# Optimization experiments

Hardware: AMD Instinct MI355X
Metric: run time of the kernel (lower is better)

## Reference

```python
import jax, jax.numpy as jnp
import numpy as np

NUM_HEADS = 16


def setup_inputs() -> dict:
    key = jax.random.key(0)
    ks = jax.random.split(key, 4)
    B, S, D = 2, 2048, 1024
    scale = 1.0 / np.sqrt(D)
    x = jax.random.normal(ks[0], (B, S, D), dtype=jnp.float32)
    Wq = jax.random.normal(ks[1], (D, D), dtype=jnp.float32) * scale
    Wk = jax.random.normal(ks[2], (D, D), dtype=jnp.float32) * scale
    Wv = jax.random.normal(ks[3], (D, D), dtype=jnp.float32) * scale
    bq = jnp.zeros((D,), dtype=jnp.float32)
    bk = jnp.zeros((D,), dtype=jnp.float32)
    bv = jnp.zeros((D,), dtype=jnp.float32)
    return {"x": x, "Wq": Wq, "bq": bq, "Wk": Wk, "bk": bk, "Wv": Wv, "bv": bv}


def _split_heads(t, H):
    B, S, D = t.shape
    return t.reshape(B, S, H, D // H).transpose(0, 2, 1, 3)  # (B,H,S,depth)


def reference(x, Wq, bq, Wk, bk, Wv, bv):
    H = NUM_HEADS
    B, S, D = x.shape
    depth = D // H
    q = _split_heads(x @ Wq + bq, H)
    k = _split_heads(x @ Wk + bk, H)
    v = _split_heads(x @ Wv + bv, H)
    # causal mask: strictly-upper-triangular ones, added as finfo.min * mask
    mask = 1.0 - jnp.tril(jnp.ones((S, S), dtype=jnp.float32))
    scores = jnp.einsum("bhqd,bhkd->bhqk", q, k) / jnp.sqrt(jnp.float32(depth))
    scores = scores + jnp.float32(np.finfo(np.float32).min) * mask
    probs = jax.nn.softmax(scores, axis=-1)
    att = jnp.einsum("bhqk,bhkd->bhqd", probs, v)
    return att.transpose(0, 2, 1, 3).reshape(B, S, D)
```

## Files before the change

### kernel.cpp

```cpp
#include <hip/hip_runtime.h>
#include <hip/hip_bf16.h>

#define B_ 2
#define S_ 2048
#define D_ 1024
#define H_ 16
#define DH 64
#define M_ (B_*S_)
#define NT_ (S_/64)

using bf16x8 = __attribute__((ext_vector_type(8))) __bf16;
using f32x4  = __attribute__((ext_vector_type(4))) float;

__device__ __forceinline__ int swz(int row) { return ((row ^ (row >> 3)) & 7) << 3; }

__device__ __forceinline__ void glds16(const __bf16* g, __bf16* l) {
#if __has_builtin(__builtin_amdgcn_global_load_lds)
  __builtin_amdgcn_global_load_lds(
      (const __attribute__((address_space(1))) unsigned int*)g,
      (__attribute__((address_space(3))) unsigned int*)l, 16, 0, 0);
#else
  *(bf16x8*)l = *(const bf16x8*)g;
#endif
}

__global__ __launch_bounds__(256) void conv_x(const float* __restrict__ x,
                                              __bf16* __restrict__ xb) {
  int idx = blockIdx.x * 256 + threadIdx.x;
  int m = idx >> 7, k = (idx & 127) * 8;
  float4 a = *(const float4*)&x[(size_t)m * D_ + k];
  float4 b = *(const float4*)&x[(size_t)m * D_ + k + 4];
  bf16x8 o;
  o[0]=(__bf16)a.x; o[1]=(__bf16)a.y; o[2]=(__bf16)a.z; o[3]=(__bf16)a.w;
  o[4]=(__bf16)b.x; o[5]=(__bf16)b.y; o[6]=(__bf16)b.z; o[7]=(__bf16)b.w;
  *(bf16x8*)&xb[(size_t)m * D_ + (k & ~63) + ((k & 63) ^ swz(m))] = o;
}

__global__ __launch_bounds__(256) void conv_w(const float* __restrict__ Wq,
                                              const float* __restrict__ Wk,
                                              const float* __restrict__ Wv,
                                              __bf16* __restrict__ wt) {
  int z = blockIdx.z;
  const float* __restrict__ W = (z == 0) ? Wq : (z == 1) ? Wk : Wv;
  __bf16* __restrict__ Wt = wt + (size_t)z * D_ * D_;
  __shared__ __bf16 Lt[64 * 66];
  int tid = threadIdx.x;
  int k0 = blockIdx.x * 64, n0 = blockIdx.y * 64;
  #pragma unroll
  for (int i = 0; i < 4; ++i) {
    int f4 = i * 256 + tid;
    int r = f4 >> 4, c4 = (f4 & 15) * 4;
    float4 v = *(const float4*)&W[(size_t)(k0 + r) * D_ + n0 + c4];
    Lt[(c4 + 0) * 66 + r] = (__bf16)v.x;
    Lt[(c4 + 1) * 66 + r] = (__bf16)v.y;
    Lt[(c4 + 2) * 66 + r] = (__bf16)v.z;
    Lt[(c4 + 3) * 66 + r] = (__bf16)v.w;
  }
  __syncthreads();
  #pragma unroll
  for (int i = 0; i < 2; ++i) {
    int idx = i * 256 + tid;
    int n = idx >> 3, kc = (idx & 7) * 8;
    int nf = n0 + n;
    bf16x8 o;
    #pragma unroll
    for (int j = 0; j < 8; ++j) o[j] = Lt[n * 66 + kc + j];
    *(bf16x8*)&Wt[(size_t)nf * D_ + k0 + (kc ^ swz(nf))] = o;
  }
}

__global__ __launch_bounds__(256) void qkv_gemm(
    const __bf16* __restrict__ xb, const __bf16* __restrict__ wt,
    const float* __restrict__ bq, const float* __restrict__ bk,
    const float* __restrict__ bv, __bf16* __restrict__ qkv) {
  int z = blockIdx.z;
  const __bf16* __restrict__ Wt = wt + (size_t)z * D_ * D_;
  const float* __restrict__ bias = (z == 0) ? bq : (z == 1) ? bk : bv;
  __bf16* __restrict__ out = qkv + (size_t)z * M_ * D_;
  const float scale = (z == 0) ? 0.125f : 1.0f;

  __shared__ __bf16 Al[128 * 64];
  __shared__ __bf16 Bl[128 * 64];

  int tid = threadIdx.x, lane = tid & 63, w = tid >> 6;
  int m0 = blockIdx.y * 128, n0 = blockIdx.x * 128;
  int wr = (w >> 1) * 64, wc = (w & 1) * 64;

  f32x4 acc[4][4] = {};

  for (int kt = 0; kt < D_ / 64; ++kt) {
    int k0 = kt * 64;
    #pragma unroll
    for (int r = 0; r < 4; ++r) {
      int e = (r * 256 + tid) * 8;
      int row = e >> 6, col = e & 63;
      glds16(&xb[(size_t)(m0 + row) * D_ + k0 + col], &Al[e]);
      glds16(&Wt[(size_t)(n0 + row) * D_ + k0 + col], &Bl[e]);
    }
    __syncthreads();

    bf16x8 af[4][2], bfr[4][2];
    #pragma unroll
    for (int mi = 0; mi < 4; ++mi) {
      int row = wr + mi * 16 + (lane & 15);
      int sr = swz(row);
      #pragma unroll
      for (int kk = 0; kk < 2; ++kk)
        af[mi][kk] = *(const bf16x8*)&Al[row * 64 + ((kk * 32 + (lane >> 4) * 8) ^ sr)];
    }
    #pragma unroll
    for (int ni = 0; ni < 4; ++ni) {
      int col = wc + ni * 16 + (lane & 15);
      int sc = swz(col);
      #pragma unroll
      for (int kk = 0; kk < 2; ++kk)
        bfr[ni][kk] = *(const bf16x8*)&Bl[col * 64 + ((kk * 32 + (lane >> 4) * 8) ^ sc)];
    }
    __builtin_amdgcn_s_setprio(1);
    #pragma unroll
    for (int kk = 0; kk < 2; ++kk)
      #pragma unroll
      for (int mi = 0; mi < 4; ++mi)
        #pragma unroll
        for (int ni = 0; ni < 4; ++ni)
          acc[mi][ni] = __builtin_amdgcn_mfma_f32_16x16x32_bf16(
              af[mi][kk], bfr[ni][kk], acc[mi][ni], 0, 0, 0);
    __builtin_amdgcn_s_setprio(0);
    __syncthreads();
  }

  #pragma unroll
  for (int mi = 0; mi < 4; ++mi) {
    #pragma unroll
    for (int ni = 0; ni < 4; ++ni) {
      int col = n0 + wc + ni * 16 + (lane & 15);
      int h = col >> 6, dh = col & 63;
      float bv_ = bias[col];
      #pragma unroll
      for (int r = 0; r < 4; ++r) {
        int row = m0 + wr + mi * 16 + (lane >> 4) * 4 + r;
        int b = row >> 11, s = row & 2047;
        out[((size_t)(b * H_ + h) * S_ + s) * DH + dh] =
            (__bf16)((acc[mi][ni][r] + bv_) * scale);
      }
    }
  }
}

__device__ __forceinline__ void attn_tile(
    const bf16x8* aq, f32x4* accO, float* mrow, float* lrow,
    const __bf16* __restrict__ Kl, const __bf16* __restrict__ Vt,
    __bf16* __restrict__ Plw, int lane, int kv0, int qbase, int diag) {
  f32x4 sf[4];
  __builtin_amdgcn_s_setprio(1);
  #pragma unroll
  for (int f = 0; f < 4; ++f) {
    f32x4 zz = {};
    int col = f * 16 + (lane & 15);
    int sc = swz(col);
    #pragma unroll
    for (int kk = 0; kk < 2; ++kk) {
      bf16x8 bk = *(const bf16x8*)&Kl[col * 64 + ((kk * 32 + (lane >> 4) * 8) ^ sc)];
      zz = __builtin_amdgcn_mfma_f32_16x16x32_bf16(aq[kk], bk, zz, 0, 0, 0);
    }
    sf[f] = zz;
  }
  __builtin_amdgcn_s_setprio(0);

  if (diag) {
    #pragma unroll
    for (int f = 0; f < 4; ++f) {
      int kvg = kv0 + f * 16 + (lane & 15);
      #pragma unroll
      for (int r = 0; r < 4; ++r) {
        int qg = qbase + (lane >> 4) * 4 + r;
        if (kvg > qg) sf[f][r] = -1e30f;
      }
    }
  }

  float alpha[4];
  #pragma unroll
  for (int r = 0; r < 4; ++r) {
    float mx = fmaxf(fmaxf(sf[0][r], sf[1][r]), fmaxf(sf[2][r], sf[3][r]));
    #pragma unroll
    for (int off = 8; off >= 1; off >>= 1)
      mx = fmaxf(mx, __shfl_xor(mx, off, 64));
    float mnew = fmaxf(mrow[r], mx);
    alpha[r] = __expf(mrow[r] - mnew);
    mrow[r] = mnew;
    float rs = 0.f;
    #pragma unroll
    for (int f = 0; f < 4; ++f) {
      float p = __expf(sf[f][r] - mnew);
      sf[f][r] = p;
      rs += p;
    }
    #pragma unroll
    for (int off = 8; off >= 1; off >>= 1)
      rs += __shfl_xor(rs, off, 64);
    lrow[r] = lrow[r] * alpha[r] + rs;
  }

  #pragma unroll
  for (int f = 0; f < 4; ++f)
    #pragma unroll
    for (int r = 0; r < 4; ++r) {
      int row = (lane >> 4) * 4 + r;
      Plw[row * 64 + ((f * 16 + (lane & 15)) ^ swz(row))] = (__bf16)sf[f][r];
    }

  #pragma unroll
  for (int f = 0; f < 4; ++f)
    #pragma unroll
    for (int r = 0; r < 4; ++r)
      accO[f][r] *= alpha[r];

  __builtin_amdgcn_s_setprio(1);
  #pragma unroll
  for (int kk = 0; kk < 2; ++kk) {
    int prow = lane & 15;
    bf16x8 pa = *(const bf16x8*)&Plw[prow * 64 + ((kk * 32 + (lane >> 4) * 8) ^ swz(prow))];
    #pragma unroll
    for (int f = 0; f < 4; ++f) {
      int vrow = f * 16 + (lane & 15);
      bf16x8 vb = *(const bf16x8*)&Vt[vrow * 64 + ((kk * 32 + (lane >> 4) * 8) ^ swz(vrow))];
      accO[f] = __builtin_amdgcn_mfma_f32_16x16x32_bf16(pa, vb, accO[f], 0, 0, 0);
    }
  }
  __builtin_amdgcn_s_setprio(0);
}

__device__ __forceinline__ void attn_out(
    const f32x4* accO, const float* lrow, float* __restrict__ out,
    int b, int h, int qbase, int lane) {
  #pragma unroll
  for (int f = 0; f < 4; ++f) {
    int dh = f * 16 + (lane & 15);
    #pragma unroll
    for (int r = 0; r < 4; ++r) {
      int qg = qbase + (lane >> 4) * 4 + r;
      out[((size_t)(b * S_ + qg)) * D_ + h * DH + dh] = accO[f][r] / lrow[r];
    }
  }
}

__global__ __launch_bounds__(256) void attn(
    const __bf16* __restrict__ Q, const __bf16* __restrict__ K,
    const __bf16* __restrict__ V, float* __restrict__ out) {
  __shared__ __bf16 Kl[64 * 64];
  __shared__ __bf16 Vt[64 * 64];
  __shared__ __bf16 Pl[4][16 * 64];

  int tid = threadIdx.x, lane = tid & 63, w = tid >> 6;
  int bx = blockIdx.x, h = blockIdx.y, b = blockIdx.z;
  int qA0 = bx * 64, qB0 = (NT_ - 1 - bx) * 64;
  size_t base = ((size_t)(b * H_ + h)) * S_ * DH;
  const __bf16* __restrict__ Qg = Q + base;
  const __bf16* __restrict__ Kg = K + base;
  const __bf16* __restrict__ Vg = V + base;

  bf16x8 aqA[2], aqB[2];
  int qra = qA0 + w * 16 + (lane & 15), qrb = qB0 + w * 16 + (lane & 15);
  #pragma unroll
  for (int kk = 0; kk < 2; ++kk) {
    aqA[kk] = *(const bf16x8*)&Qg[(size_t)qra * DH + kk * 32 + (lane >> 4) * 8];
    aqB[kk] = *(const bf16x8*)&Qg[(size_t)qrb * DH + kk * 32 + (lane >> 4) * 8];
  }

  f32x4 accA[4] = {}, accB[4] = {};
  float mA[4], lA[4], mB[4], lB[4];
  #pragma unroll
  for (int r = 0; r < 4; ++r) { mA[r] = mB[r] = -1e30f; lA[r] = lB[r] = 0.f; }

  const int ktA = bx, ktB = NT_ - 1 - bx;
  for (int kt = 0; kt <= ktB; ++kt) {
    int kv0 = kt * 64;
    #pragma unroll
    for (int i = 0; i < 2; ++i) {
      int e = (i * 256 + tid) * 8;
      int kv = e >> 6, d0 = e & 63;
      bf16x8 k8 = *(const bf16x8*)&Kg[(size_t)(kv0 + kv) * DH + d0];
      *(bf16x8*)&Kl[kv * 64 + (d0 ^ swz(kv))] = k8;
      bf16x8 v8 = *(const bf16x8*)&Vg[(size_t)(kv0 + kv) * DH + d0];
      #pragma unroll
      for (int j = 0; j < 8; ++j) {
        int row = d0 + j;
        Vt[row * 64 + (kv ^ swz(row))] = v8[j];
      }
    }
    __syncthreads();

    attn_tile(aqB, accB, mB, lB, Kl, Vt, Pl[w], lane, kv0, qB0 + w * 16, kt == ktB);
    if (kt <= ktA)
      attn_tile(aqA, accA, mA, lA, Kl, Vt, Pl[w], lane, kv0, qA0 + w * 16, kt == ktA);
    __syncthreads();
  }

  attn_out(accA, lA, out, b, h, qA0 + w * 16, lane);
  attn_out(accB, lB, out, b, h, qB0 + w * 16, lane);
}

extern "C" void kernel_launch(void* const* d_in, const int* in_sizes, int n_in,
                              void* d_out, int out_size, void* d_ws, size_t ws_size,
                              hipStream_t stream) {
  const float* x  = (const float*)d_in[0];
  const float* Wq = (const float*)d_in[1];
  const float* bq = (const float*)d_in[2];
  const float* Wk = (const float*)d_in[3];
  const float* bk = (const float*)d_in[4];
  const float* Wv = (const float*)d_in[5];
  const float* bv = (const float*)d_in[6];
  float* out = (float*)d_out;

  __bf16* xb  = (__bf16*)d_ws;
  __bf16* wt  = xb + (size_t)M_ * D_;
  __bf16* qkv = wt + (size_t)3 * D_ * D_;
  __bf16* wsq = qkv;
  __bf16* wsk = qkv + (size_t)M_ * D_;
  __bf16* wsv = qkv + (size_t)2 * M_ * D_;

  conv_x<<<(M_ * (D_ / 8)) / 256, 256, 0, stream>>>(x, xb);
  conv_w<<<dim3(D_ / 64, D_ / 64, 3), 256, 0, stream>>>(Wq, Wk, Wv, wt);
  qkv_gemm<<<dim3(D_ / 128, M_ / 128, 3), 256, 0, stream>>>(xb, wt, bq, bk, bv, qkv);
  attn<<<dim3(NT_ / 2, H_, B_), 256, 0, stream>>>(wsq, wsk, wsv, out);
}
```

Before: 204.8 us.

## Double attention KV tile to 128 and prefetch next K/V tile into registers

The attention kernel now processes 128 keys per iteration instead of 64. Scores, the softmax reduction and the P·V MFMA loop are widened to match, and the shared-memory K, Vt and P buffers are resized. The next tile's K and V are loaded into registers while the current tile is being computed, so global-load latency overlaps with MFMA work and half as many block barriers are needed. The s_setprio hints are also dropped from the projection GEMM. In exchange, register and LDS use go up, which may lower occupancy, and the coarser causal tiles do more masked work on the diagonal.

```diff
diff --git a/kernel.cpp b/kernel.cpp
--- a/kernel.cpp
+++ b/kernel.cpp
@@ -8,6 +8,7 @@
 #define DH 64
 #define M_ (B_*S_)
 #define NT_ (S_/64)
+#define KVB 128
 
 using bf16x8 = __attribute__((ext_vector_type(8))) __bf16;
 using f32x4  = __attribute__((ext_vector_type(4))) float;
@@ -116,7 +117,6 @@
       for (int kk = 0; kk < 2; ++kk)
         bfr[ni][kk] = *(const bf16x8*)&Bl[col * 64 + ((kk * 32 + (lane >> 4) * 8) ^ sc)];
     }
-    __builtin_amdgcn_s_setprio(1);
     #pragma unroll
     for (int kk = 0; kk < 2; ++kk)
       #pragma unroll
@@ -125,7 +125,6 @@
         for (int ni = 0; ni < 4; ++ni)
           acc[mi][ni] = __builtin_amdgcn_mfma_f32_16x16x32_bf16(
               af[mi][kk], bfr[ni][kk], acc[mi][ni], 0, 0, 0);
-    __builtin_amdgcn_s_setprio(0);
     __syncthreads();
   }
 
@@ -147,14 +146,14 @@
   }
 }
 
-__device__ __forceinline__ void attn_tile(
+__device__ __forceinline__ void attn_tile8(
     const bf16x8* aq, f32x4* accO, float* mrow, float* lrow,
     const __bf16* __restrict__ Kl, const __bf16* __restrict__ Vt,
-    __bf16* __restrict__ Plw, int lane, int kv0, int qbase, int diag) {
-  f32x4 sf[4];
+    __bf16* __restrict__ Plw, int lane, int kv0, int qbase, bool diag) {
+  f32x4 sf[8];
   __builtin_amdgcn_s_setprio(1);
   #pragma unroll
-  for (int f = 0; f < 4; ++f) {
+  for (int f = 0; f < 8; ++f) {
     f32x4 zz = {};
     int col = f * 16 + (lane & 15);
     int sc = swz(col);
@@ -169,7 +168,7 @@
 
   if (diag) {
     #pragma unroll
-    for (int f = 0; f < 4; ++f) {
+    for (int f = 0; f < 8; ++f) {
       int kvg = kv0 + f * 16 + (lane & 15);
       #pragma unroll
       for (int r = 0; r < 4; ++r) {
@@ -182,7 +181,9 @@
   float alpha[4];
   #pragma unroll
   for (int r = 0; r < 4; ++r) {
-    float mx = fmaxf(fmaxf(sf[0][r], sf[1][r]), fmaxf(sf[2][r], sf[3][r]));
+    float mx = sf[0][r];
+    #pragma unroll
+    for (int f = 1; f < 8; ++f) mx = fmaxf(mx, sf[f][r]);
     #pragma unroll
     for (int off = 8; off >= 1; off >>= 1)
       mx = fmaxf(mx, __shfl_xor(mx, off, 64));
@@ -191,7 +192,7 @@
     mrow[r] = mnew;
     float rs = 0.f;
     #pragma unroll
-    for (int f = 0; f < 4; ++f) {
+    for (int f = 0; f < 8; ++f) {
       float p = __expf(sf[f][r] - mnew);
       sf[f][r] = p;
       rs += p;
@@ -203,11 +204,11 @@
   }
 
   #pragma unroll
-  for (int f = 0; f < 4; ++f)
+  for (int f = 0; f < 8; ++f)
     #pragma unroll
     for (int r = 0; r < 4; ++r) {
       int row = (lane >> 4) * 4 + r;
-      Plw[row * 64 + ((f * 16 + (lane & 15)) ^ swz(row))] = (__bf16)sf[f][r];
+      Plw[row * KVB + ((f * 16 + (lane & 15)) ^ swz(row))] = (__bf16)sf[f][r];
     }
 
   #pragma unroll
@@ -218,13 +219,13 @@
 
   __builtin_amdgcn_s_setprio(1);
   #pragma unroll
-  for (int kk = 0; kk < 2; ++kk) {
+  for (int kk = 0; kk < 4; ++kk) {
     int prow = lane & 15;
-    bf16x8 pa = *(const bf16x8*)&Plw[prow * 64 + ((kk * 32 + (lane >> 4) * 8) ^ swz(prow))];
+    bf16x8 pa = *(const bf16x8*)&Plw[prow * KVB + ((kk * 32 + (lane >> 4) * 8) ^ swz(prow))];
     #pragma unroll
     for (int f = 0; f < 4; ++f) {
       int vrow = f * 16 + (lane & 15);
-      bf16x8 vb = *(const bf16x8*)&Vt[vrow * 64 + ((kk * 32 + (lane >> 4) * 8) ^ swz(vrow))];
+      bf16x8 vb = *(const bf16x8*)&Vt[vrow * KVB + ((kk * 32 + (lane >> 4) * 8) ^ swz(vrow))];
       accO[f] = __builtin_amdgcn_mfma_f32_16x16x32_bf16(pa, vb, accO[f], 0, 0, 0);
     }
   }
@@ -248,9 +249,9 @@
 __global__ __launch_bounds__(256) void attn(
     const __bf16* __restrict__ Q, const __bf16* __restrict__ K,
     const __bf16* __restrict__ V, float* __restrict__ out) {
-  __shared__ __bf16 Kl[64 * 64];
-  __shared__ __bf16 Vt[64 * 64];
-  __shared__ __bf16 Pl[4][16 * 64];
+  __shared__ __bf16 Kl[KVB * 64];
+  __shared__ __bf16 Vt[64 * KVB];
+  __shared__ __bf16 Pl[4][16 * KVB];
 
   int tid = threadIdx.x, lane = tid & 63, w = tid >> 6;
   int bx = blockIdx.x, h = blockIdx.y, b = blockIdx.z;
@@ -273,27 +274,49 @@
   #pragma unroll
   for (int r = 0; r < 4; ++r) { mA[r] = mB[r] = -1e30f; lA[r] = lB[r] = 0.f; }
 
-  const int ktA = bx, ktB = NT_ - 1 - bx;
-  for (int kt = 0; kt <= ktB; ++kt) {
-    int kv0 = kt * 64;
-    #pragma unroll
-    for (int i = 0; i < 2; ++i) {
+  const int ktAmax = (qA0 + 63) >> 7;
+  const int ktBmax = (qB0 + 63) >> 7;
+
+  bf16x8 kreg[4], vreg[4];
+  #pragma unroll
+  for (int i = 0; i < 4; ++i) {
+    int e = (i * 256 + tid) * 8;
+    int kv = e >> 6, d0 = e & 63;
+    kreg[i] = *(const bf16x8*)&Kg[(size_t)kv * DH + d0];
+    vreg[i] = *(const bf16x8*)&Vg[(size_t)kv * DH + d0];
+  }
+
+  for (int kt = 0; kt <= ktBmax; ++kt) {
+    int kv0 = kt * KVB;
+    #pragma unroll
+    for (int i = 0; i < 4; ++i) {
       int e = (i * 256 + tid) * 8;
       int kv = e >> 6, d0 = e & 63;
-      bf16x8 k8 = *(const bf16x8*)&Kg[(size_t)(kv0 + kv) * DH + d0];
-      *(bf16x8*)&Kl[kv * 64 + (d0 ^ swz(kv))] = k8;
-      bf16x8 v8 = *(const bf16x8*)&Vg[(size_t)(kv0 + kv) * DH + d0];
+      *(bf16x8*)&Kl[kv * 64 + (d0 ^ swz(kv))] = kreg[i];
       #pragma unroll
       for (int j = 0; j < 8; ++j) {
         int row = d0 + j;
-        Vt[row * 64 + (kv ^ swz(row))] = v8[j];
+        Vt[row * KVB + (kv ^ swz(row))] = vreg[i][j];
       }
     }
     __syncthreads();
 
-    attn_tile(aqB, accB, mB, lB, Kl, Vt, Pl[w], lane, kv0, qB0 + w * 16, kt == ktB);
-    if (kt <= ktA)
-      attn_tile(aqA, accA, mA, lA, Kl, Vt, Pl[w], lane, kv0, qA0 + w * 16, kt == ktA);
+    if (kt < ktBmax) {
+      int kvn = kv0 + KVB;
+      #pragma unroll
+      for (int i = 0; i < 4; ++i) {
+        int e = (i * 256 + tid) * 8;
+        int kv = e >> 6, d0 = e & 63;
+        kreg[i] = *(const bf16x8*)&Kg[(size_t)(kvn + kv) * DH + d0];
+        vreg[i] = *(const bf16x8*)&Vg[(size_t)(kvn + kv) * DH + d0];
+      }
+    }
+
+    attn_tile8(aqB, accB, mB, lB, Kl, Vt, Pl[w], lane, kv0, qB0 + w * 16,
+               kv0 + KVB - 1 > qB0);
+    if (kt <= ktAmax)
+      attn_tile8(aqA, accA, mA, lA, Kl, Vt, Pl[w], lane, kv0, qA0 + w * 16,
+                 kv0 + KVB - 1 > qA0);
     __syncthreads();
   }
 
```

Measured after the change: 229.9 us. 1.12x slower.

## Enlarge QKV GEMM tiles to 256x256 with double-buffered LDS staging

Applied to the files above, without the earlier changes.

The QKV projection GEMM moves from 128x128 tiles with 256 threads to 256x256 tiles with 512 threads. Each wave now computes a 128x64 sub-tile with 8x4 MFMA accumulators. LDS is double-buffered so the global-to-LDS load of the next K slice is issued before computing the current one, leaving one barrier per iteration. This is meant to raise operand reuse per LDS byte and hide load latency. The cost is only 192 workgroups for the whole GEMM, large register and LDS use per block, and the removal of the s_setprio hints.

```diff
diff --git a/kernel.cpp b/kernel.cpp
--- a/kernel.cpp
+++ b/kernel.cpp
@@ -69,7 +69,12 @@
   }
 }
 
-__global__ __launch_bounds__(256) void qkv_gemm(
+#define BM 256
+#define BN 256
+#define BK 64
+#define NKT (D_/BK)
+
+__global__ __launch_bounds__(512, 2) void qkv_gemm(
     const __bf16* __restrict__ xb, const __bf16* __restrict__ wt,
     const float* __restrict__ bq, const float* __restrict__ bk,
     const float* __restrict__ bv, __bf16* __restrict__ qkv) {
@@ -79,58 +84,63 @@
   __bf16* __restrict__ out = qkv + (size_t)z * M_ * D_;
   const float scale = (z == 0) ? 0.125f : 1.0f;
 
-  __shared__ __bf16 Al[128 * 64];
-  __shared__ __bf16 Bl[128 * 64];
+  __shared__ __bf16 Al[2][BM * BK];
+  __shared__ __bf16 Bl[2][BM * BK];
 
   int tid = threadIdx.x, lane = tid & 63, w = tid >> 6;
-  int m0 = blockIdx.y * 128, n0 = blockIdx.x * 128;
-  int wr = (w >> 1) * 64, wc = (w & 1) * 64;
-
-  f32x4 acc[4][4] = {};
-
-  for (int kt = 0; kt < D_ / 64; ++kt) {
-    int k0 = kt * 64;
-    #pragma unroll
-    for (int r = 0; r < 4; ++r) {
-      int e = (r * 256 + tid) * 8;
-      int row = e >> 6, col = e & 63;
-      glds16(&xb[(size_t)(m0 + row) * D_ + k0 + col], &Al[e]);
-      glds16(&Wt[(size_t)(n0 + row) * D_ + k0 + col], &Bl[e]);
-    }
-    __syncthreads();
-
-    bf16x8 af[4][2], bfr[4][2];
-    #pragma unroll
-    for (int mi = 0; mi < 4; ++mi) {
-      int row = wr + mi * 16 + (lane & 15);
-      int sr = swz(row);
-      #pragma unroll
-      for (int kk = 0; kk < 2; ++kk)
-        af[mi][kk] = *(const bf16x8*)&Al[row * 64 + ((kk * 32 + (lane >> 4) * 8) ^ sr)];
-    }
-    #pragma unroll
-    for (int ni = 0; ni < 4; ++ni) {
-      int col = wc + ni * 16 + (lane & 15);
-      int sc = swz(col);
-      #pragma unroll
-      for (int kk = 0; kk < 2; ++kk)
-        bfr[ni][kk] = *(const bf16x8*)&Bl[col * 64 + ((kk * 32 + (lane >> 4) * 8) ^ sc)];
-    }
-    __builtin_amdgcn_s_setprio(1);
-    #pragma unroll
-    for (int kk = 0; kk < 2; ++kk)
-      #pragma unroll
-      for (int mi = 0; mi < 4; ++mi)
+  int m0 = blockIdx.y * BM, n0 = blockIdx.x * BN;
+  int wr = (w >> 2) * 128;
+  int wc = (w & 3) * 64;
+
+  f32x4 acc[8][4] = {};
+
+#define STAGE(buf, kt)                                                        \
+  {                                                                           \
+    int k0 = (kt) * BK;                                                       \
+    _Pragma("unroll")                                                         \
+    for (int r = 0; r < 4; ++r) {                                             \
+      int e = (r * 512 + tid) * 8;                                            \
+      int row = e >> 6, col = e & 63;                                         \
+      glds16(&xb[(size_t)(m0 + row) * D_ + k0 + col], &Al[buf][e]);           \
+      glds16(&Wt[(size_t)(n0 + row) * D_ + k0 + col], &Bl[buf][e]);           \
+    }                                                                         \
+  }
+
+  STAGE(0, 0);
+  __syncthreads();
+
+  int cur = 0;
+  for (int kt = 0; kt < NKT; ++kt) {
+    if (kt + 1 < NKT) STAGE(cur ^ 1, kt + 1);
+    #pragma unroll
+    for (int kk = 0; kk < 2; ++kk) {
+      bf16x8 af[8], bfr[4];
+      #pragma unroll
+      for (int mi = 0; mi < 8; ++mi) {
+        int row = wr + mi * 16 + (lane & 15);
+        af[mi] = *(const bf16x8*)&Al[cur][row * 64 +
+                 ((kk * 32 + (lane >> 4) * 8) ^ swz(row))];
+      }
+      #pragma unroll
+      for (int ni = 0; ni < 4; ++ni) {
+        int col = wc + ni * 16 + (lane & 15);
+        bfr[ni] = *(const bf16x8*)&Bl[cur][col * 64 +
+                  ((kk * 32 + (lane >> 4) * 8) ^ swz(col))];
+      }
+      #pragma unroll
+      for (int mi = 0; mi < 8; ++mi)
         #pragma unroll
         for (int ni = 0; ni < 4; ++ni)
           acc[mi][ni] = __builtin_amdgcn_mfma_f32_16x16x32_bf16(
-              af[mi][kk], bfr[ni][kk], acc[mi][ni], 0, 0, 0);
-    __builtin_amdgcn_s_setprio(0);
+              af[mi], bfr[ni], acc[mi][ni], 0, 0, 0);
+    }
     __syncthreads();
-  }
-
-  #pragma unroll
-  for (int mi = 0; mi < 4; ++mi) {
+    cur ^= 1;
+  }
+#undef STAGE
+
+  #pragma unroll
+  for (int mi = 0; mi < 8; ++mi) {
     #pragma unroll
     for (int ni = 0; ni < 4; ++ni) {
       int col = n0 + wc + ni * 16 + (lane & 15);
@@ -322,6 +332,6 @@
 
   conv_x<<<(M_ * (D_ / 8)) / 256, 256, 0, stream>>>(x, xb);
   conv_w<<<dim3(D_ / 64, D_ / 64, 3), 256, 0, stream>>>(Wq, Wk, Wv, wt);
-  qkv_gemm<<<dim3(D_ / 128, M_ / 128, 3), 256, 0, stream>>>(xb, wt, bq, bk, bv, qkv);
+  qkv_gemm<<<dim3(D_ / BN, M_ / BM, 3), 512, 0, stream>>>(xb, wt, bq, bk, bv, qkv);
   attn<<<dim3(NT_ / 2, H_, B_), 256, 0, stream>>>(wsq, wsk, wsv, out);
 }
```

Measured after the change: 198.9 us. 1.03x faster.
